# Performance work log

Hardware: AMD Instinct MI355X
Metric: run time of the kernel (lower is better)

## Reference

```python
import jax, jax.numpy as jnp
import numpy as np

CONF_TH = 0.6      # confidence_threshold
IOU_TH = 0.45      # iou_threshold
MAX_WH = 4096.0    # class offset for class-aware NMS (agnostic=False)
TOP_K = 1024       # fixed candidate cap (analog of max_nms, jit-static)
MAX_DET = 300      # max detections per image
NC = 80
AGNOSTIC = False


def setup_inputs() -> dict:
    key = jax.random.key(0)
    k1, k2 = jax.random.split(key)
    prediction = jax.random.uniform(k1, (16, 25200, 85), dtype=jnp.float32)
    logits = jax.random.uniform(k2, (16, 25200, 80), dtype=jnp.float32)
    return {"prediction": prediction, "logits": logits}


def xywh2xyxy(b):
    cx, cy, w, h = b[:, 0], b[:, 1], b[:, 2], b[:, 3]
    return jnp.stack([cx - w * 0.5, cy - h * 0.5, cx + w * 0.5, cy + h * 0.5], axis=-1)


def box_iou(a, b):
    # a: [K,4], b: [K,4] in xyxy -> [K,K] IoU
    area_a = (a[:, 2] - a[:, 0]) * (a[:, 3] - a[:, 1])
    area_b = (b[:, 2] - b[:, 0]) * (b[:, 3] - b[:, 1])
    lt = jnp.maximum(a[:, None, :2], b[None, :, :2])
    rb = jnp.minimum(a[:, None, 2:], b[None, :, 2:])
    wh = jnp.clip(rb - lt, 0.0)
    inter = wh[..., 0] * wh[..., 1]
    return inter / (area_a[:, None] + area_b[None, :] - inter + 1e-9)


def _greedy_keep(iou, valid):
    # iou: [K,K] on score-descending boxes; valid: [K] bool
    K = iou.shape[0]
    ar = jnp.arange(K)

    def step(suppressed, i):
        keep_i = valid[i] & ~suppressed[i]
        suppressed = suppressed | (keep_i & (iou[i] > IOU_TH) & (ar > i))
        return suppressed, keep_i

    _, keep = jax.lax.scan(step, jnp.zeros((K,), dtype=bool), ar)
    return keep


def _nms_image(pred, logit):
    # pred: [N, 5+nc], logit: [N, nc]
    obj = pred[:, 4]
    cls_scores = pred[:, 5:] * obj[:, None]          # x[:,5:] *= x[:,4:5]
    conf = jnp.max(cls_scores, axis=-1)              # best-class confidence
    cls = jnp.argmax(cls_scores, axis=-1)
    valid = (obj > CONF_TH) & (conf > CONF_TH)       # xc gate + conf gate
    box = xywh2xyxy(pred[:, :4])

    score = jnp.where(valid, conf, -1.0)
    top_scores, idx = jax.lax.top_k(score, TOP_K)    # descending-score candidates
    box_k = box[idx]                                  # [K,4] original boxes
    cls_k = cls[idx]
    logit_k = logit[idx]
    valid_k = top_scores > CONF_TH

    # class-aware offset (agnostic=False) for NMS only
    off = 0.0 if AGNOSTIC else MAX_WH
    nms_boxes = box_k + cls_k[:, None].astype(box_k.dtype) * off

    iou = box_iou(nms_boxes, nms_boxes)
    keep = _greedy_keep(iou, valid_k)

    kept_score = jnp.where(keep, top_scores, -1.0)
    sel_score, sel = jax.lax.top_k(kept_score, MAX_DET)
    out_valid = sel_score > CONF_TH

    det = jnp.concatenate(
        [box_k[sel], top_scores[sel][:, None], cls_k[sel][:, None].astype(jnp.float32)],
        axis=1,
    )  # [max_det, 6] = [xyxy, conf, cls]
    det = jnp.where(out_valid[:, None], det, 0.0)
    logits_out = jnp.where(out_valid[:, None], logit_k[sel], 0.0)  # [max_det, nc]
    return det, out_valid, logits_out


def reference(prediction, logits):
    det, valid, logits_out = jax.vmap(_nms_image)(prediction, logits)
    return det, valid, logits_out
```

## Files before the change

### kernel.cpp

```cpp
#include <hip/hip_runtime.h>
#include <stdint.h>

#define CONF_THR 0.6f
#define IOU_THR  0.45f
#define MAX_WH_F 4096.0f
#define TOPK     1024
#define MAX_DET  300
#define NCLS     80
#define ROW      85
#define APB      128
#define NMS_P    32

typedef unsigned int u32;
typedef unsigned long long u64;

__device__ __forceinline__ u32 f2s(float f) {
    u32 b = __float_as_uint(f);
    return b ^ ((u32)((int)b >> 31) | 0x80000000u);
}
__device__ __forceinline__ float s2f(u32 k) {
    u32 b = (k & 0x80000000u) ? (k ^ 0x80000000u) : ~k;
    return __uint_as_float(b);
}

__global__ __launch_bounds__(256) void k_score(const float* __restrict__ pred,
        u32* __restrict__ key, u32* __restrict__ cls, int NA) {
#pragma clang fp contract(off)
    int img = blockIdx.y;
    int a0 = blockIdx.x * APB;
    int count = min(APB, NA - a0);
    if (count <= 0) return;
    size_t baseoff = ((size_t)img * NA + a0) * ROW;
    const float* base = pred + baseoff;
    __shared__ __align__(16) float tile[APB * ROW];
    int nfloat = count * ROW;
    if ((baseoff & 3) == 0) {
        int nvec = nfloat >> 2;
        const float4* b4 = (const float4*)base;
        float4* t4 = (float4*)tile;
        for (int i = threadIdx.x; i < nvec; i += blockDim.x) t4[i] = b4[i];
        for (int i = (nvec << 2) + threadIdx.x; i < nfloat; i += blockDim.x)
            tile[i] = base[i];
    } else {
        for (int i = threadIdx.x; i < nfloat; i += blockDim.x) tile[i] = base[i];
    }
    __syncthreads();
    int t = threadIdx.x;
    if (t < count) {
        const float* r = tile + t * ROW;
        float obj = r[4];
        float maxv = -1.0f; int cl = 0;
        for (int j = 0; j < NCLS; ++j) {
            float v = r[5 + j] * obj;
            if (v > maxv) { maxv = v; cl = j; }
        }
        bool valid = (obj > CONF_THR) && (maxv > CONF_THR);
        float score = valid ? maxv : -1.0f;
        size_t g = (size_t)img * NA + a0 + t;
        key[g] = f2s(score);
        cls[g] = (u32)cl;
    }
}

__global__ __launch_bounds__(1024) void k_topk(const u32* __restrict__ key,
        u32* __restrict__ top_idx, float* __restrict__ top_score, int NA) {
    int img = blockIdx.x;
    const u32* kb = key + (size_t)img * NA;
    __shared__ u32 hist[256];
    __shared__ u32 sfx[256];
    __shared__ int sh_d;
    __shared__ u32 sh_t;
    __shared__ u32 gcnt;
    __shared__ u64 skey[TOPK];
    int tid = threadIdx.x;
    int lane = tid & 63;
    u64 lanemask = (1ull << lane) - 1ull;
    u32 prefix = 0, target = TOPK;
    for (int level = 0; level < 4; ++level) {
        int shift = 24 - 8 * level;
        if (tid < 256) hist[tid] = 0;
        __syncthreads();
        for (int idx0 = 0; idx0 < NA; idx0 += 1024) {
            int idx = idx0 + tid;
            bool inb = idx < NA;
            u32 k = inb ? kb[idx] : 0u;
            bool in = inb && ((level == 0) || ((k >> (shift + 8)) == prefix));
            u32 d = (k >> shift) & 0xFFu;
            u64 peers = __ballot(in);
#pragma unroll
            for (int bit = 0; bit < 8; ++bit) {
                u64 bb = __ballot((d >> bit) & 1u);
                peers &= ((d >> bit) & 1u) ? bb : ~bb;
            }
            if (in) {
                int leader = (int)(__ffsll((long long)peers) - 1);
                if (lane == leader) atomicAdd(&hist[d], (u32)__popcll(peers));
            }
        }
        __syncthreads();
        if (tid < 256) sfx[tid] = hist[tid];
        __syncthreads();
        for (int off = 1; off < 256; off <<= 1) {
            u32 v = 0;
            if (tid < 256) {
                v = sfx[tid];
                if (tid + off < 256) v += sfx[tid + off];
            }
            __syncthreads();
            if (tid < 256) sfx[tid] = v;
            __syncthreads();
        }
        if (tid < 256) {
            u32 S = sfx[tid];
            u32 Snext = (tid == 255) ? 0u : sfx[tid + 1];
            if (S >= target && Snext < target) { sh_d = tid; sh_t = target - Snext; }
        }
        __syncthreads();
        prefix = (prefix << 8) | (u32)sh_d;
        target = sh_t;
        __syncthreads();
    }
    u32 cutv = prefix;
    u32 R = target;
    u32 T = hist[cutv & 0xFFu];
    if (tid == 0) gcnt = 0;
    __syncthreads();
    bool takeTies = (T == R);
    for (int c0 = 0; c0 < NA; c0 += 1024) {
        int idx = c0 + tid;
        bool inb = idx < NA;
        u32 k = inb ? kb[idx] : 0u;
        bool put = inb && ((k > cutv) || (takeTies && k == cutv));
        u64 ball = __ballot(put);
        if (ball) {
            int leader = (int)(__ffsll((long long)ball) - 1);
            u32 base = 0;
            if (lane == leader) base = atomicAdd(&gcnt, (u32)__popcll(ball));
            base = __shfl(base, leader);
            if (put)
                skey[base + (u32)__popcll(ball & lanemask)] =
                    ((u64)k << 32) | (u64)(u32)(NA - 1 - idx);
        }
    }
    __syncthreads();
    if (!takeTies) {
        u32 G = gcnt;
        if (tid < 64) {
            u32 cnt = 0;
            for (int c0 = 0; c0 < NA; c0 += 64) {
                int idx = c0 + tid;
                bool ist = (idx < NA) && (kb[idx] == cutv);
                u64 ball = __ballot(ist);
                u32 rank = cnt + (u32)__popcll(ball & lanemask);
                if (ist && rank < R)
                    skey[G + rank] = ((u64)cutv << 32) | (u64)(u32)(NA - 1 - idx);
                cnt += (u32)__popcll(ball);
                if (cnt >= R) break;
            }
        }
        __syncthreads();
    }
    for (int k2 = 2; k2 <= TOPK; k2 <<= 1) {
        for (int j = k2 >> 1; j > 0; j >>= 1) {
            int i = tid, ixj = i ^ j;
            if (ixj > i) {
                u64 a = skey[i], b = skey[ixj];
                bool desc = ((i & k2) == 0);
                if ((a < b) == desc) { skey[i] = b; skey[ixj] = a; }
            }
            __syncthreads();
        }
    }
    u64 kk = skey[tid];
    u32 aidx = (u32)(NA - 1) - (u32)(kk & 0xFFFFFFFFull);
    top_idx[img * TOPK + tid] = aidx;
    top_score[img * TOPK + tid] = s2f((u32)(kk >> 32));
}

__global__ void k_prep(const float* __restrict__ pred, const u32* __restrict__ cls,
        const u32* __restrict__ top_idx,
        float* __restrict__ boxk, float* __restrict__ nmsbox,
        float* __restrict__ clsf, int NA) {
#pragma clang fp contract(off)
    int img = blockIdx.y;
    int t = blockIdx.x * blockDim.x + threadIdx.x;
    if (t >= TOPK) return;
    int g = img * TOPK + t;
    u32 aidx = top_idx[g];
    const float* r = pred + ((size_t)img * NA + aidx) * ROW;
    float cx = r[0], cy = r[1], w = r[2], h = r[3];
    float hw = w * 0.5f, hh = h * 0.5f;
    float x1 = cx - hw, y1 = cy - hh, x2 = cx + hw, y2 = cy + hh;
    u32 c = cls[(size_t)img * NA + aidx];
    float off = (float)c * MAX_WH_F;
    boxk[g * 4 + 0] = x1; boxk[g * 4 + 1] = y1;
    boxk[g * 4 + 2] = x2; boxk[g * 4 + 3] = y2;
    nmsbox[g * 4 + 0] = x1 + off; nmsbox[g * 4 + 1] = y1 + off;
    nmsbox[g * 4 + 2] = x2 + off; nmsbox[g * 4 + 3] = y2 + off;
    clsf[g] = (float)c;
}

__global__ __launch_bounds__(1024) void k_mask(const float* __restrict__ nmsbox,
        u64* __restrict__ mask) {
#pragma clang fp contract(off)
    int img = blockIdx.y;
    __shared__ float bx[TOPK + 32], by[TOPK + 32], bX[TOPK + 32], bY[TOPK + 32], ar[TOPK + 32];
    int tid = threadIdx.x;
    {
        const float4* nb = (const float4*)(nmsbox + (size_t)img * TOPK * 4);
        float4 b = nb[tid];
        int pi = tid + (tid >> 5);
        bx[pi] = b.x; by[pi] = b.y; bX[pi] = b.z; bY[pi] = b.w;
        ar[pi] = (b.z - b.x) * (b.w - b.y);
    }
    __syncthreads();
    int i = blockIdx.x * 64 + (tid >> 4);
    int w = tid & 15;
    int pi = i + (i >> 5);
    float ax = bx[pi], ay = by[pi], aX = bX[pi], aY = bY[pi], aa = ar[pi];
    u64 bits = 0;
    for (int jj = 0; jj < 64; ++jj) {
        int j = (w << 6) + jj;
        if (j > i) {
            int pj = j + (j >> 5);
            float ltx = fmaxf(ax, bx[pj]);
            float lty = fmaxf(ay, by[pj]);
            float rbx = fminf(aX, bX[pj]);
            float rby = fminf(aY, bY[pj]);
            float ww = fmaxf(rbx - ltx, 0.0f);
            float hh = fmaxf(rby - lty, 0.0f);
            float inter = ww * hh;
            float denom = ((aa + ar[pj]) - inter) + 1e-9f;
            float iou = inter / denom;
            if (iou > IOU_THR) bits |= (1ull << jj);
        }
    }
    mask[((size_t)img * TOPK + i) * 16 + w] = bits;
}

__global__ __launch_bounds__(64) void k_nms(const u64* __restrict__ mask,
        const float* __restrict__ top_score,
        u32* __restrict__ sel, u32* __restrict__ selcnt) {
    int img = blockIdx.x;
    int lane = threadIdx.x;
    const u64* mrow = mask + (size_t)img * TOPK * 16;
    int cnt = 0;
    for (int k = 0; k < TOPK / 64; ++k) {
        float s = top_score[img * TOPK + k * 64 + lane];
        cnt += (s > CONF_THR) ? 1 : 0;
    }
    for (int off = 32; off > 0; off >>= 1) cnt += __shfl_down(cnt, off);
    int nvalid = __shfl(cnt, 0);

    bool ld = lane < 16;
    u64 rem = 0;
    u64 buf[NMS_P];
#pragma unroll
    for (int k = 0; k < NMS_P; ++k)
        buf[k] = ld ? mrow[(size_t)k * 16 + lane] : 0ull;
    int kept = 0;
    for (int base = 0; base < TOPK; base += NMS_P) {
        if (base >= nvalid || kept >= MAX_DET) break;
#pragma unroll
        for (int k = 0; k < NMS_P; ++k) {
            int i = base + k;
            u64 roww = buf[k];
            int pf = i + NMS_P;
            buf[k] = (ld && pf < TOPK) ? mrow[(size_t)pf * 16 + lane] : 0ull;
            if (i < nvalid && kept < MAX_DET) {
                bool notsup = (lane == (i >> 6)) && !((rem >> (i & 63)) & 1ull);
                if (__ballot(notsup) != 0ull) {
                    if (lane == 0) sel[img * MAX_DET + kept] = (u32)i;
                    rem |= roww;
                    ++kept;
                }
            }
        }
    }
    if (lane == 0) selcnt[img] = (u32)kept;
}

__global__ void k_out(const float* __restrict__ logits,
        const u32* __restrict__ top_idx, const float* __restrict__ top_score,
        const float* __restrict__ boxk, const float* __restrict__ clsf,
        const u32* __restrict__ sel, const u32* __restrict__ selcnt,
        float* __restrict__ out, int NA, int B) {
    int img = blockIdx.y;
    int t = blockIdx.x;
    int tid = threadIdx.x;
    u32 K = selcnt[img];
    size_t detoff = ((size_t)img * MAX_DET + t) * 6;
    size_t voff = (size_t)B * MAX_DET * 6 + (size_t)img * MAX_DET + t;
    size_t loff = (size_t)B * MAX_DET * 7 + ((size_t)img * MAX_DET + t) * NCLS;
    if ((u32)t < K) {
        int slot = (int)sel[img * MAX_DET + t];
        int g = img * TOPK + slot;
        u32 aidx = top_idx[g];
        if (tid < NCLS)      out[loff + tid] = logits[((size_t)img * NA + aidx) * NCLS + tid];
        else if (tid < 84)   out[detoff + (tid - 80)] = boxk[(size_t)g * 4 + (tid - 80)];
        else if (tid == 84)  out[detoff + 4] = top_score[g];
        else if (tid == 85)  out[detoff + 5] = clsf[g];
        else if (tid == 86)  out[voff] = 1.0f;
    } else {
        if (tid < NCLS)      out[loff + tid] = 0.0f;
        else if (tid < 86)   out[detoff + (tid - 80)] = 0.0f;
        else if (tid == 86)  out[voff] = 0.0f;
    }
}

extern "C" void kernel_launch(void* const* d_in, const int* in_sizes, int n_in,
                              void* d_out, int out_size, void* d_ws, size_t ws_size,
                              hipStream_t stream) {
    const float* pred = (const float*)d_in[0];
    const float* logits = (const float*)d_in[1];
    float* out = (float*)d_out;
    const int B = out_size / (MAX_DET * (6 + 1 + NCLS));
    const int NA = in_sizes[0] / (B * ROW);

    char* p = (char*)d_ws;
    auto alloc = [&](size_t bytes) -> void* {
        void* r = (void*)p;
        p += (bytes + 255) & ~(size_t)255;
        return r;
    };
    u32* key       = (u32*)alloc((size_t)B * NA * 4);
    u32* cls       = (u32*)alloc((size_t)B * NA * 4);
    u32* top_idx   = (u32*)alloc((size_t)B * TOPK * 4);
    float* top_scr = (float*)alloc((size_t)B * TOPK * 4);
    float* boxk    = (float*)alloc((size_t)B * TOPK * 16);
    float* nmsbox  = (float*)alloc((size_t)B * TOPK * 16);
    float* clsf    = (float*)alloc((size_t)B * TOPK * 4);
    u64* mask      = (u64*)alloc((size_t)B * TOPK * 16 * 8);
    u32* sel       = (u32*)alloc((size_t)B * MAX_DET * 4);
    u32* selcnt    = (u32*)alloc((size_t)B * 4);

    k_score<<<dim3((NA + APB - 1) / APB, B), 256, 0, stream>>>(pred, key, cls, NA);
    k_topk<<<dim3(B), 1024, 0, stream>>>(key, top_idx, top_scr, NA);
    k_prep<<<dim3(TOPK / 256, B), 256, 0, stream>>>(pred, cls, top_idx, boxk, nmsbox, clsf, NA);
    k_mask<<<dim3(TOPK / 64, B), 1024, 0, stream>>>(nmsbox, mask);
    k_nms<<<dim3(B), 64, 0, stream>>>(mask, top_scr, sel, selcnt);
    k_out<<<dim3(MAX_DET, B), 128, 0, stream>>>(logits, top_idx, top_scr, boxk, clsf,
                                                sel, selcnt, out, NA, B);
}
```

Measured before the change: 454.8 us.

## Fuse prep into topk, per-wave histograms, fewer barriers, restructure NMS scan

The radix-select histogram now uses per-wave shared histograms, with plain atomics after the first level, and a wave-level shuffle scan replaces the barrier-heavy block scan. The bitonic sort skips barriers for strides under 64, which stay inside one wave. The prep kernel is folded into the topk kernel, removing one launch. The NMS kernel runs 1024 threads: the extra waves read the mask buffer to warm the cache, while one wave does the greedy scan with a 16-deep prefetch ring, records kept bits per 64-box word, and writes the selection list afterwards. Risks include the dummy cache-warming reads and the larger per-wave shared histograms.

```diff
diff --git a/kernel.cpp b/kernel.cpp
--- a/kernel.cpp
+++ b/kernel.cpp
@@ -9,7 +9,7 @@
 #define NCLS     80
 #define ROW      85
 #define APB      128
-#define NMS_P    32
+#define RING     16
 
 typedef unsigned int u32;
 typedef unsigned long long u64;
@@ -63,22 +63,26 @@
 }
 
 __global__ __launch_bounds__(1024) void k_topk(const u32* __restrict__ key,
-        u32* __restrict__ top_idx, float* __restrict__ top_score, int NA) {
+        const float* __restrict__ pred, const u32* __restrict__ cls,
+        u32* __restrict__ top_idx, float* __restrict__ top_score,
+        float* __restrict__ boxk, float* __restrict__ nmsbox,
+        float* __restrict__ clsf, int NA) {
+#pragma clang fp contract(off)
     int img = blockIdx.x;
     const u32* kb = key + (size_t)img * NA;
-    __shared__ u32 hist[256];
-    __shared__ u32 sfx[256];
+    __shared__ u32 whist[16 * 256];
+    __shared__ u32 hfin[256];
     __shared__ int sh_d;
     __shared__ u32 sh_t;
     __shared__ u32 gcnt;
     __shared__ u64 skey[TOPK];
     int tid = threadIdx.x;
-    int lane = tid & 63;
+    int wid = tid >> 6, lane = tid & 63;
     u64 lanemask = (1ull << lane) - 1ull;
     u32 prefix = 0, target = TOPK;
     for (int level = 0; level < 4; ++level) {
         int shift = 24 - 8 * level;
-        if (tid < 256) hist[tid] = 0;
+        for (int i = tid; i < 16 * 256; i += 1024) whist[i] = 0;
         __syncthreads();
         for (int idx0 = 0; idx0 < NA; idx0 += 1024) {
             int idx = idx0 + tid;
@@ -86,43 +90,54 @@
             u32 k = inb ? kb[idx] : 0u;
             bool in = inb && ((level == 0) || ((k >> (shift + 8)) == prefix));
             u32 d = (k >> shift) & 0xFFu;
-            u64 peers = __ballot(in);
+            if (level == 0) {
+                u64 peers = __ballot(in);
 #pragma unroll
-            for (int bit = 0; bit < 8; ++bit) {
-                u64 bb = __ballot((d >> bit) & 1u);
-                peers &= ((d >> bit) & 1u) ? bb : ~bb;
-            }
-            if (in) {
-                int leader = (int)(__ffsll((long long)peers) - 1);
-                if (lane == leader) atomicAdd(&hist[d], (u32)__popcll(peers));
-            }
-        }
-        __syncthreads();
-        if (tid < 256) sfx[tid] = hist[tid];
-        __syncthreads();
-        for (int off = 1; off < 256; off <<= 1) {
-            u32 v = 0;
-            if (tid < 256) {
-                v = sfx[tid];
-                if (tid + off < 256) v += sfx[tid + off];
-            }
-            __syncthreads();
-            if (tid < 256) sfx[tid] = v;
-            __syncthreads();
-        }
+                for (int bit = 0; bit < 8; ++bit) {
+                    u64 bb = __ballot((d >> bit) & 1u);
+                    peers &= ((d >> bit) & 1u) ? bb : ~bb;
+                }
+                if (in) {
+                    int leader = (int)(__ffsll((long long)peers) - 1);
+                    if (lane == leader)
+                        atomicAdd(&whist[(wid << 8) | d], (u32)__popcll(peers));
+                }
+            } else {
+                if (in) atomicAdd(&whist[(wid << 8) | d], 1u);
+            }
+        }
+        __syncthreads();
         if (tid < 256) {
-            u32 S = sfx[tid];
-            u32 Snext = (tid == 255) ? 0u : sfx[tid + 1];
-            if (S >= target && Snext < target) { sh_d = tid; sh_t = target - Snext; }
+            u32 s = 0;
+#pragma unroll
+            for (int w = 0; w < 16; ++w) s += whist[(w << 8) | tid];
+            hfin[tid] = s;
+        }
+        __syncthreads();
+        if (tid < 64) {
+            u32 h0 = hfin[4 * tid], h1 = hfin[4 * tid + 1];
+            u32 h2 = hfin[4 * tid + 2], h3 = hfin[4 * tid + 3];
+            u32 s = h0 + h1 + h2 + h3;
+            u32 t = s;
+#pragma unroll
+            for (int off = 1; off < 64; off <<= 1) {
+                u32 o = (u32)__shfl_down((int)t, off);
+                if (tid + off < 64) t += o;
+            }
+            u32 S0 = t, S1 = t - h0, S2 = S1 - h1, S3 = S2 - h2, S4 = t - s;
+            u32 tg = target;
+            if (S0 >= tg && S1 < tg) { sh_d = 4 * tid;     sh_t = tg - S1; }
+            if (S1 >= tg && S2 < tg) { sh_d = 4 * tid + 1; sh_t = tg - S2; }
+            if (S2 >= tg && S3 < tg) { sh_d = 4 * tid + 2; sh_t = tg - S3; }
+            if (S3 >= tg && S4 < tg) { sh_d = 4 * tid + 3; sh_t = tg - S4; }
         }
         __syncthreads();
         prefix = (prefix << 8) | (u32)sh_d;
         target = sh_t;
-        __syncthreads();
     }
     u32 cutv = prefix;
     u32 R = target;
-    u32 T = hist[cutv & 0xFFu];
+    u32 T = hfin[cutv & 0xFFu];
     if (tid == 0) gcnt = 0;
     __syncthreads();
     bool takeTies = (T == R);
@@ -160,36 +175,29 @@
         }
         __syncthreads();
     }
+    int jprev = 0;
     for (int k2 = 2; k2 <= TOPK; k2 <<= 1) {
         for (int j = k2 >> 1; j > 0; j >>= 1) {
+            if (j >= 64 || jprev >= 64) __syncthreads();
             int i = tid, ixj = i ^ j;
             if (ixj > i) {
                 u64 a = skey[i], b = skey[ixj];
                 bool desc = ((i & k2) == 0);
                 if ((a < b) == desc) { skey[i] = b; skey[ixj] = a; }
             }
-            __syncthreads();
-        }
-    }
+            jprev = j;
+        }
+    }
+    __syncthreads();
     u64 kk = skey[tid];
     u32 aidx = (u32)(NA - 1) - (u32)(kk & 0xFFFFFFFFull);
-    top_idx[img * TOPK + tid] = aidx;
-    top_score[img * TOPK + tid] = s2f((u32)(kk >> 32));
-}
-
-__global__ void k_prep(const float* __restrict__ pred, const u32* __restrict__ cls,
-        const u32* __restrict__ top_idx,
-        float* __restrict__ boxk, float* __restrict__ nmsbox,
-        float* __restrict__ clsf, int NA) {
-#pragma clang fp contract(off)
-    int img = blockIdx.y;
-    int t = blockIdx.x * blockDim.x + threadIdx.x;
-    if (t >= TOPK) return;
-    int g = img * TOPK + t;
-    u32 aidx = top_idx[g];
+    float sc = s2f((u32)(kk >> 32));
+    int g = img * TOPK + tid;
+    top_idx[g] = aidx;
+    top_score[g] = sc;
     const float* r = pred + ((size_t)img * NA + aidx) * ROW;
-    float cx = r[0], cy = r[1], w = r[2], h = r[3];
-    float hw = w * 0.5f, hh = h * 0.5f;
+    float cx = r[0], cy = r[1], w4 = r[2], h4 = r[3];
+    float hw = w4 * 0.5f, hh = h4 * 0.5f;
     float x1 = cx - hw, y1 = cy - hh, x2 = cx + hw, y2 = cy + hh;
     u32 c = cls[(size_t)img * NA + aidx];
     float off = (float)c * MAX_WH_F;
@@ -238,46 +246,77 @@
     mask[((size_t)img * TOPK + i) * 16 + w] = bits;
 }
 
-__global__ __launch_bounds__(64) void k_nms(const u64* __restrict__ mask,
+__global__ __launch_bounds__(1024) void k_nms(const u64* __restrict__ mask,
         const float* __restrict__ top_score,
-        u32* __restrict__ sel, u32* __restrict__ selcnt) {
+        u32* __restrict__ sel, u32* __restrict__ selcnt, u32* __restrict__ dummy) {
+    __shared__ u32 s_nvalid;
+    __shared__ u64 keepw[16];
     int img = blockIdx.x;
-    int lane = threadIdx.x;
+    int tid = threadIdx.x;
+    int lane = tid & 63;
+    if (tid == 0) s_nvalid = 0;
+    if (tid < 16) keepw[tid] = 0;
+    __syncthreads();
+    {
+        float s = top_score[img * TOPK + tid];
+        u64 b = __ballot(s > CONF_THR);
+        if (lane == 0) atomicAdd(&s_nvalid, (u32)__popcll(b));
+    }
+    __syncthreads();
     const u64* mrow = mask + (size_t)img * TOPK * 16;
-    int cnt = 0;
-    for (int k = 0; k < TOPK / 64; ++k) {
-        float s = top_score[img * TOPK + k * 64 + lane];
-        cnt += (s > CONF_THR) ? 1 : 0;
-    }
-    for (int off = 32; off > 0; off >>= 1) cnt += __shfl_down(cnt, off);
-    int nvalid = __shfl(cnt, 0);
-
+    if (tid >= 64) {
+        const uint4* m16 = (const uint4*)mrow;
+        u32 acc = 0;
+        for (int i = tid - 64; i < 8192; i += 960) {
+            uint4 v = m16[i];
+            acc ^= v.x ^ v.y ^ v.z ^ v.w;
+        }
+        if (acc == 0xDEADBEEFu) *dummy = acc;
+        return;
+    }
+    int nvalid = (int)s_nvalid;
     bool ld = lane < 16;
     u64 rem = 0;
-    u64 buf[NMS_P];
+    u64 pf[RING];
 #pragma unroll
-    for (int k = 0; k < NMS_P; ++k)
-        buf[k] = ld ? mrow[(size_t)k * 16 + lane] : 0ull;
-    int kept = 0;
-    for (int base = 0; base < TOPK; base += NMS_P) {
-        if (base >= nvalid || kept >= MAX_DET) break;
-#pragma unroll
-        for (int k = 0; k < NMS_P; ++k) {
-            int i = base + k;
-            u64 roww = buf[k];
-            int pf = i + NMS_P;
-            buf[k] = (ld && pf < TOPK) ? mrow[(size_t)pf * 16 + lane] : 0ull;
-            if (i < nvalid && kept < MAX_DET) {
-                bool notsup = (lane == (i >> 6)) && !((rem >> (i & 63)) & 1ull);
-                if (__ballot(notsup) != 0ull) {
-                    if (lane == 0) sel[img * MAX_DET + kept] = (u32)i;
-                    rem |= roww;
-                    ++kept;
-                }
-            }
-        }
-    }
-    if (lane == 0) selcnt[img] = (u32)kept;
+    for (int k = 0; k < RING; ++k)
+        pf[k] = ld ? mrow[(size_t)k * 16 + lane] : 0ull;
+    int nblk = (nvalid + 63) >> 6;
+    int kept_total = 0;
+    for (int blk = 0; blk < nblk; ++blk) {
+        u64 kw = 0;
+        int base = blk << 6;
+#pragma unroll 16
+        for (int t = 0; t < 64; ++t) {
+            int i = base + t;
+            u64 roww = pf[i & (RING - 1)];
+            int nx = i + RING;
+            pf[i & (RING - 1)] = (ld && nx < TOPK) ? mrow[(size_t)nx * 16 + lane] : 0ull;
+            bool notsup = (lane == (i >> 6)) && !((rem >> (i & 63)) & 1ull);
+            if (__ballot(notsup) != 0ull) {
+                rem |= roww;
+                kw |= (1ull << t);
+            }
+        }
+        int over = nvalid - base;
+        if (over < 64) kw &= (over <= 0) ? 0ull : ((1ull << over) - 1ull);
+        if (lane == 0) keepw[blk] = kw;
+        kept_total += (int)__popcll(kw);
+        if (kept_total >= MAX_DET) break;
+    }
+    if (lane < 16) {
+        u64 kw = keepw[lane];
+        u32 rank = 0;
+        for (int m = 0; m < 16; ++m)
+            if (m < lane) rank += (u32)__popcll(keepw[m]);
+        while (kw) {
+            int b = (int)__ffsll((long long)kw) - 1;
+            if (rank < MAX_DET) sel[img * MAX_DET + rank] = (u32)((lane << 6) + b);
+            ++rank;
+            kw &= kw - 1;
+        }
+    }
+    if (lane == 0) selcnt[img] = (u32)min(kept_total, MAX_DET);
 }
 
 __global__ void k_out(const float* __restrict__ logits,
@@ -332,13 +371,14 @@
     float* clsf    = (float*)alloc((size_t)B * TOPK * 4);
     u64* mask      = (u64*)alloc((size_t)B * TOPK * 16 * 8);
     u32* sel       = (u32*)alloc((size_t)B * MAX_DET * 4);
-    u32* selcnt    = (u32*)alloc((size_t)B * 4);
+    u32* selcnt    = (u32*)alloc((size_t)(B + 1) * 4);
+    u32* dummy     = selcnt + B;
 
     k_score<<<dim3((NA + APB - 1) / APB, B), 256, 0, stream>>>(pred, key, cls, NA);
-    k_topk<<<dim3(B), 1024, 0, stream>>>(key, top_idx, top_scr, NA);
-    k_prep<<<dim3(TOPK / 256, B), 256, 0, stream>>>(pred, cls, top_idx, boxk, nmsbox, clsf, NA);
+    k_topk<<<dim3(B), 1024, 0, stream>>>(key, pred, cls, top_idx, top_scr,
+                                         boxk, nmsbox, clsf, NA);
     k_mask<<<dim3(TOPK / 64, B), 1024, 0, stream>>>(nmsbox, mask);
-    k_nms<<<dim3(B), 64, 0, stream>>>(mask, top_scr, sel, selcnt);
+    k_nms<<<dim3(B), 1024, 0, stream>>>(mask, top_scr, sel, selcnt, dummy);
     k_out<<<dim3(MAX_DET, B), 128, 0, stream>>>(logits, top_idx, top_scr, boxk, clsf,
                                                 sel, selcnt, out, NA, B);
 }
```

After: 368.1 us. -19.1%, faster.
